# Kernel tuning notes

Measured on AMD Instinct MI355X. Metric: run time of the kernel, lower is better.

## Reference

```python
import jax, jax.numpy as jnp
import numpy as np

NC = 10      # num_classes
HID = 64     # hidden_layer_dim
CIN = 512    # input_channels
THRESH = 100 # _LABEL2MASK_THRESHOL


def setup_inputs() -> dict:
    key = jax.random.key(0)
    k = jax.random.split(key, 5)
    B, h, w = 4, 60, 80
    feature1 = jax.random.normal(k[0], (B, CIN, h, w), jnp.float32)
    feature2 = jax.random.normal(k[1], (B, CIN, h // 2, w // 2), jnp.float32)
    s_in = (2.0 / CIN) ** 0.5   # kaiming_normal_ fan_in for 1x1 conv
    s_h = (2.0 / HID) ** 0.5
    w1 = jax.random.normal(k[2], (HID, CIN), jnp.float32) * s_in
    b1 = jnp.zeros((HID,), jnp.float32)
    w2 = jax.random.normal(k[3], (HID, CIN), jnp.float32) * s_in
    b2 = jnp.zeros((HID,), jnp.float32)
    w3 = jax.random.normal(k[4], (NC + 1, HID), jnp.float32) * s_h
    b3 = jnp.zeros((NC + 1,), jnp.float32)
    return {"feature1": feature1, "feature2": feature2,
            "w1": w1, "b1": b1, "w2": w2, "b2": b2, "w3": w3, "b3": b3}


def _resize_bilinear(x, H, W):
    # torch nn.Upsample(mode='bilinear', align_corners=False) ~ jax.image.resize bilinear
    B, C = x.shape[0], x.shape[1]
    return jax.image.resize(x, (B, C, H, W), method="bilinear")


def _label2bbx(seg):
    # Vectorized replacement of the batch x class Python loop: fused masked
    # min/max reductions per (batch, class). Classes 1..NC-1, class 0 skipped,
    # exactly as in the original. Fixed output shape (B*(NC-1), 6); rows with
    # pixel count < THRESH are filled with -1 (jit-compatible padding).
    B, H, W = seg.shape
    cls = jnp.arange(1, NC)                                   # (NC-1,)
    mask = seg[:, None, :, :] == cls[None, :, None, None]     # (B, NC-1, H, W)
    xs = jnp.arange(W)
    ys = jnp.arange(H)
    count = mask.sum(axis=(-2, -1))                           # (B, NC-1)
    xmin = jnp.min(jnp.where(mask, xs[None, None, None, :], W), axis=(-2, -1))
    xmax = jnp.max(jnp.where(mask, xs[None, None, None, :], -1), axis=(-2, -1))
    ymin = jnp.min(jnp.where(mask, ys[None, None, :, None], H), axis=(-2, -1))
    ymax = jnp.max(jnp.where(mask, ys[None, None, :, None], -1), axis=(-2, -1))
    bids = jnp.broadcast_to(jnp.arange(B)[:, None], (B, NC - 1))
    clsb = jnp.broadcast_to(cls[None, :], (B, NC - 1))
    bbx = jnp.stack([bids, xmin, ymin, xmax, ymax, clsb], axis=-1)  # (B, NC-1, 6)
    valid = (count >= THRESH)[..., None]
    return jnp.where(valid, bbx, -1).reshape(B * (NC - 1), 6)


def reference(feature1, feature2, w1, b1, w2, b2, w3, b3):
    # 1x1 convs expressed as channel GEMMs
    f1 = jax.nn.relu(jnp.einsum('bchw,oc->bohw', feature1, w1) + b1[None, :, None, None])
    f2 = jax.nn.relu(jnp.einsum('bchw,oc->bohw', feature2, w2) + b2[None, :, None, None])
    h, w = feature1.shape[2], feature1.shape[3]
    f2 = _resize_bilinear(f2, h, w)           # Upsample x2
    inter = f1 + f2
    up = _resize_bilinear(inter, 8 * h, 8 * w)  # Upsample x8
    logits = jax.nn.relu(jnp.einsum('bchw,oc->bohw', up, w3) + b3[None, :, None, None])
    probability = jax.nn.softmax(logits, axis=1)   # Softmax2d = softmax over C
    segmentation = jnp.argmax(probability, axis=1)  # (B, H, W)
    bbx = _label2bbx(segmentation)
    return probability, segmentation, bbx
```

## Files before the change

kernel.cpp:

```cpp
#include <hip/hip_runtime.h>

#define DEVINL __device__ __forceinline__

namespace {

constexpr int NB   = 4;
constexpr int CINv = 512;
constexpr int HIDv = 64;
constexpr int NCl  = 11;
constexpr int h1v = 60, w1v = 80;
constexpr int h2v = 30, w2v = 40;
constexpr int Hf = 480, Wf = 640;
constexpr int PPB1 = h1v * w1v;
constexpr int PPB2 = h2v * w2v;
constexpr int NP1 = NB * PPB1;
constexpr int NP2 = NB * PPB2;
constexpr int PPBF = Hf * Wf;
constexpr int NPF = NB * PPBF;

constexpr size_t WS_P1  = 0;
constexpr size_t WS_P2  = WS_P1 + 2ull * HIDv * NP1;
constexpr size_t WS_Z   = WS_P2 + 2ull * HIDv * NP2;
constexpr size_t WS_BBX = WS_Z + (size_t)NB * NCl * PPB1;

constexpr size_t OUT_SEG = (size_t)NB * NCl * PPBF;
constexpr size_t OUT_BBX = OUT_SEG + (size_t)NPF;

DEVINL int iclamp(int v, int lo, int hi) { return v < lo ? lo : (v > hi ? hi : v); }

template <int PPB>
DEVINL void gemm_tile(const float* __restrict__ F, const float* __restrict__ Wt,
                      float* __restrict__ P, int npix, int tile, int khalf,
                      float* A_lds , float* W_lds ) {
  const int t = threadIdx.x;
  const int pg = t & 15;
  const int og = t >> 4;
  const int gp0 = tile * 64;
  const int c0 = khalf * 256;

  float acc[4][4];
#pragma unroll
  for (int i = 0; i < 4; ++i)
#pragma unroll
    for (int j = 0; j < 4; ++j) acc[i][j] = 0.f;

  for (int kb = 0; kb < 8; ++kb) {
    const int cb = c0 + kb * 32;
    __syncthreads();
#pragma unroll
    for (int e = 0; e < 8; ++e) {
      int idx = e * 256 + t;
      int cc = idx >> 6, px = idx & 63;
      int gp = gp0 + px;
      int b = gp / PPB, pb = gp % PPB;
      A_lds[idx] = F[((size_t)b * CINv + (cb + cc)) * PPB + pb];
    }
#pragma unroll
    for (int e = 0; e < 8; ++e) {
      int idx = e * 256 + t;
      int o = idx >> 5, cc = idx & 31;
      W_lds[cc * 68 + o] = Wt[o * CINv + cb + cc];
    }
    __syncthreads();
#pragma unroll
    for (int cc = 0; cc < 32; ++cc) {
      float4 a = *reinterpret_cast<const float4*>(&A_lds[cc * 64 + pg * 4]);
      float4 w = *reinterpret_cast<const float4*>(&W_lds[cc * 68 + og * 4]);
      float av[4] = {a.x, a.y, a.z, a.w};
      float wv[4] = {w.x, w.y, w.z, w.w};
#pragma unroll
      for (int i = 0; i < 4; ++i)
#pragma unroll
        for (int j = 0; j < 4; ++j)
          acc[i][j] = fmaf(av[i], wv[j], acc[i][j]);
    }
  }
#pragma unroll
  for (int j = 0; j < 4; ++j) {
    int o = og * 4 + j;
    float4 v;
    v.x = acc[0][j]; v.y = acc[1][j]; v.z = acc[2][j]; v.w = acc[3][j];
    *reinterpret_cast<float4*>(&P[((size_t)khalf * HIDv + o) * npix + gp0 + pg * 4]) = v;
  }
}

__global__ __launch_bounds__(256) void k_gemm(const float* __restrict__ f1,
                                              const float* __restrict__ f2,
                                              const float* __restrict__ w1,
                                              const float* __restrict__ w2,
                                              float* __restrict__ ws) {
  __shared__ float A_lds[32 * 64];
  __shared__ float W_lds[32 * 68];
  const int bid = blockIdx.x;

  if (bid == 0 && threadIdx.x < 180) {
    int f = threadIdx.x % 5;
    int v = (f == 0) ? 0 : ((f == 1 || f == 3) ? 0x7fffffff : (int)0x80000000);
    reinterpret_cast<int*>(ws + WS_BBX)[threadIdx.x] = v;
  }

  if (bid < 600) {
    gemm_tile<PPB1>(f1, w1, ws + WS_P1, NP1, bid >> 1, bid & 1, A_lds, W_lds);
  } else {
    int tt = bid - 600;
    gemm_tile<PPB2>(f2, w2, ws + WS_P2, NP2, tt >> 1, tt & 1, A_lds, W_lds);
  }
}

__global__ __launch_bounds__(256) void k_combine_z(const float* __restrict__ ws_ro,
                                                   float* __restrict__ ws,
                                                   const float* __restrict__ b1,
                                                   const float* __restrict__ b2,
                                                   const float* __restrict__ w3,
                                                   const float* __restrict__ b3) {
  __shared__ float inter[64 * 64];
  const int t = threadIdx.x;
  const int pxl = t & 63;
  const int qi = t >> 6;
  const int gp = blockIdx.x * 64 + pxl;
  const int b = gp / PPB1, pb = gp % PPB1;
  const int y = pb / w1v, x = pb % w1v;

  const float sx = x * 0.5f - 0.25f;
  const float x0f = floorf(sx);
  const float fx = sx - x0f;
  const int ix0 = iclamp((int)x0f, 0, w2v - 1);
  const int ix1 = iclamp((int)x0f + 1, 0, w2v - 1);
  const float sy = y * 0.5f - 0.25f;
  const float y0f = floorf(sy);
  const float fy = sy - y0f;
  const int iy0 = iclamp((int)y0f, 0, h2v - 1);
  const int iy1 = iclamp((int)y0f + 1, 0, h2v - 1);

  const float* p1 = ws_ro + WS_P1;
  const float* p2 = ws_ro + WS_P2;
  const int base2 = b * PPB2;
  const int i00 = base2 + iy0 * w2v + ix0;
  const int i01 = base2 + iy0 * w2v + ix1;
  const int i10 = base2 + iy1 * w2v + ix0;
  const int i11 = base2 + iy1 * w2v + ix1;

#pragma unroll
  for (int cc = 0; cc < 16; ++cc) {
    const int ch = qi * 16 + cc;
    float v = p1[(size_t)ch * NP1 + gp] + p1[(size_t)(HIDv + ch) * NP1 + gp] + b1[ch];
    v = fmaxf(v, 0.f);
    const float* pa = p2 + (size_t)ch * NP2;
    const float* pbp = p2 + (size_t)(HIDv + ch) * NP2;
    const float bb = b2[ch];
    float v00 = fmaxf(pa[i00] + pbp[i00] + bb, 0.f);
    float v01 = fmaxf(pa[i01] + pbp[i01] + bb, 0.f);
    float v10 = fmaxf(pa[i10] + pbp[i10] + bb, 0.f);
    float v11 = fmaxf(pa[i11] + pbp[i11] + bb, 0.f);
    float top = v00 + fx * (v01 - v00);
    float bot = v10 + fx * (v11 - v10);
    v += top + fy * (bot - top);
    inter[ch * 64 + pxl] = v;
  }
  __syncthreads();

  const int o0 = qi * 3;
  const int ocnt = (qi == 3) ? 2 : 3;
  float* z = ws + WS_Z;
  for (int oo = 0; oo < ocnt; ++oo) {
    const int o = o0 + oo;
    float acc = b3[o];
#pragma unroll
    for (int ch = 0; ch < 64; ++ch)
      acc = fmaf(inter[ch * 64 + pxl], w3[o * HIDv + ch], acc);
    z[((size_t)b * NCl + o) * PPB1 + pb] = acc;
  }
}

__global__ __launch_bounds__(256) void k_up_softmax(const float* __restrict__ ws,
                                                    float* __restrict__ out,
                                                    int* __restrict__ bbxAcc) {
  __shared__ int sCnt[10], sXmin[10], sXmax[10], sYmin[10], sYmax[10];
  const int t = threadIdx.x;
  if (t < 10) {
    sCnt[t] = 0;
    sXmin[t] = 0x7fffffff; sXmax[t] = (int)0x80000000;
    sYmin[t] = 0x7fffffff; sYmax[t] = (int)0x80000000;
  }
  __syncthreads();

  const unsigned fp = ((unsigned)blockIdx.x * 256u + (unsigned)t) * 4u;
  const int b = fp / PPBF;
  const int r = fp % PPBF;
  const int Y = r / Wf, X = r % Wf;

  const float sy = (Y + 0.5f) * 0.125f - 0.5f;
  const float y0f = floorf(sy);
  const float fy = sy - y0f;
  const int iy0 = iclamp((int)y0f, 0, h1v - 1);
  const int iy1 = iclamp((int)y0f + 1, 0, h1v - 1);

  const float sx0 = (X + 0.5f) * 0.125f - 0.5f;
  const float x0f = floorf(sx0);
  const int ix0 = iclamp((int)x0f, 0, w1v - 1);
  const int ix1 = iclamp((int)x0f + 1, 0, w1v - 1);
  float fxk[4];
#pragma unroll
  for (int k = 0; k < 4; ++k) fxk[k] = (X + k + 0.5f) * 0.125f - 0.5f - x0f;

  const float* zb = ws + WS_Z + (size_t)b * NCl * PPB1;
  float lg[NCl][4];
#pragma unroll
  for (int c = 0; c < NCl; ++c) {
    const float* zc = zb + (size_t)c * PPB1;
    float v00 = zc[iy0 * w1v + ix0], v01 = zc[iy0 * w1v + ix1];
    float v10 = zc[iy1 * w1v + ix0], v11 = zc[iy1 * w1v + ix1];
    float l0 = v00 + fy * (v10 - v00);
    float l1 = v01 + fy * (v11 - v01);
#pragma unroll
    for (int k = 0; k < 4; ++k)
      lg[c][k] = fmaxf(l0 + fxk[k] * (l1 - l0), 0.f);
  }

  int bestc[4];
#pragma unroll
  for (int k = 0; k < 4; ++k) {
    float m = lg[0][k];
#pragma unroll
    for (int c = 1; c < NCl; ++c) m = fmaxf(m, lg[c][k]);
    float s = 0.f;
#pragma unroll
    for (int c = 0; c < NCl; ++c) {
      float e = __expf(lg[c][k] - m);
      lg[c][k] = e;
      s += e;
    }
    const float inv = 1.0f / s;
    float bp = -1.f;
    int bi = 0;
#pragma unroll
    for (int c = 0; c < NCl; ++c) {
      float p = lg[c][k] * inv;
      lg[c][k] = p;
      if (p > bp) { bp = p; bi = c; }
    }
    bestc[k] = bi;
  }

  float* prob = out + (size_t)b * NCl * PPBF;
#pragma unroll
  for (int c = 0; c < NCl; ++c) {
    float4 v;
    v.x = lg[c][0]; v.y = lg[c][1]; v.z = lg[c][2]; v.w = lg[c][3];
    *reinterpret_cast<float4*>(&prob[(size_t)c * PPBF + r]) = v;
  }
  {
    float4 v;
    v.x = (float)bestc[0]; v.y = (float)bestc[1];
    v.z = (float)bestc[2]; v.w = (float)bestc[3];
    *reinterpret_cast<float4*>(&out[OUT_SEG + fp]) = v;
  }

  for (int c = 1; c <= 9; ++c) {
    int cnt = 0, mnx = 0x7fffffff, mxx = (int)0x80000000;
#pragma unroll
    for (int k = 0; k < 4; ++k)
      if (bestc[k] == c) { ++cnt; mnx = min(mnx, X + k); mxx = max(mxx, X + k); }
    if (cnt) {
      atomicAdd(&sCnt[c], cnt);
      atomicMin(&sXmin[c], mnx);
      atomicMax(&sXmax[c], mxx);
      atomicMin(&sYmin[c], Y);
      atomicMax(&sYmax[c], Y);
    }
  }
  __syncthreads();
  if (t >= 1 && t <= 9 && sCnt[t] > 0) {
    int* e = bbxAcc + (b * 9 + (t - 1)) * 5;
    atomicAdd(e + 0, sCnt[t]);
    atomicMin(e + 1, sXmin[t]);
    atomicMax(e + 2, sXmax[t]);
    atomicMin(e + 3, sYmin[t]);
    atomicMax(e + 4, sYmax[t]);
  }
}

__global__ void k_bbx_final(const int* __restrict__ acc, float* __restrict__ out) {
  const int t = threadIdx.x;
  if (t >= 36) return;
  const int* e = acc + t * 5;
  float* o = out + OUT_BBX + t * 6;
  if (e[0] >= 100) {
    o[0] = (float)(t / 9);
    o[1] = (float)e[1];
    o[2] = (float)e[3];
    o[3] = (float)e[2];
    o[4] = (float)e[4];
    o[5] = (float)(t % 9 + 1);
  } else {
    for (int i = 0; i < 6; ++i) o[i] = -1.f;
  }
}

}

extern "C" void kernel_launch(void* const* d_in, const int* in_sizes, int n_in,
                              void* d_out, int out_size, void* d_ws, size_t ws_size,
                              hipStream_t stream) {
  const float* f1 = (const float*)d_in[0];
  const float* f2 = (const float*)d_in[1];
  const float* w1 = (const float*)d_in[2];
  const float* b1 = (const float*)d_in[3];
  const float* w2 = (const float*)d_in[4];
  const float* b2 = (const float*)d_in[5];
  const float* w3 = (const float*)d_in[6];
  const float* b3 = (const float*)d_in[7];
  float* out = (float*)d_out;
  float* ws = (float*)d_ws;

  hipLaunchKernelGGL(k_gemm, dim3(750), dim3(256), 0, stream, f1, f2, w1, w2, ws);
  hipLaunchKernelGGL(k_combine_z, dim3(300), dim3(256), 0, stream, ws, ws, b1, b2, w3, b3);
  hipLaunchKernelGGL(k_up_softmax, dim3(1200), dim3(256), 0, stream, ws, out,
                     (int*)(ws + WS_BBX));
  hipLaunchKernelGGL(k_bbx_final, dim3(1), dim3(64), 0, stream,
                     (const int*)(ws + WS_BBX), out);
}
```

Baseline: 85.72 us.

## Tile upsample-softmax blocks in 2D and stage low-res logits in LDS

Each block of the final upsample+softmax kernel now covers a 128x8 pixel tile. The block first loads the 11-channel 3x18 low-resolution logit neighbourhood into shared memory, and bilinear taps then read from LDS instead of scattered global loads. The argmax is taken on the pre-softmax logits rather than on the normalised probabilities, and the reciprocal uses the hardware rcp builtin. The cost is an extra LDS fill and barrier per block, plus slightly different rounding and tie behaviour.

```diff
diff --git a/kernel.cpp b/kernel.cpp
--- a/kernel.cpp
+++ b/kernel.cpp
@@ -175,41 +175,55 @@
 __global__ __launch_bounds__(256) void k_up_softmax(const float* __restrict__ ws,
                                                     float* __restrict__ out,
                                                     int* __restrict__ bbxAcc) {
+  constexpr int ZR = 3, ZC = 18, ZN = NCl * ZR * ZC;
+  __shared__ float zt[ZN];
   __shared__ int sCnt[10], sXmin[10], sXmax[10], sYmin[10], sYmax[10];
+
   const int t = threadIdx.x;
+  const int tile = blockIdx.x;
+  const int tx = tile % 5;
+  const int ty = (tile / 5) % 60;
+  const int b  = tile / 300;
+
+  const int base_x = tx * 16 - 1;
+  const int base_y = ty - 1;
+
   if (t < 10) {
     sCnt[t] = 0;
     sXmin[t] = 0x7fffffff; sXmax[t] = (int)0x80000000;
     sYmin[t] = 0x7fffffff; sYmax[t] = (int)0x80000000;
   }
+  const float* zb = ws + WS_Z + (size_t)b * NCl * PPB1;
+  for (int e = t; e < ZN; e += 256) {
+    int ch = e / (ZR * ZC);
+    int rc = e % (ZR * ZC);
+    int row = rc / ZC, col = rc % ZC;
+    int gr = iclamp(base_y + row, 0, h1v - 1);
+    int gc = iclamp(base_x + col, 0, w1v - 1);
+    zt[e] = zb[(size_t)ch * PPB1 + gr * w1v + gc];
+  }
   __syncthreads();
 
-  const unsigned fp = ((unsigned)blockIdx.x * 256u + (unsigned)t) * 4u;
-  const int b = fp / PPBF;
-  const int r = fp % PPBF;
-  const int Y = r / Wf, X = r % Wf;
-
-  const float sy = (Y + 0.5f) * 0.125f - 0.5f;
-  const float y0f = floorf(sy);
-  const float fy = sy - y0f;
-  const int iy0 = iclamp((int)y0f, 0, h1v - 1);
-  const int iy1 = iclamp((int)y0f + 1, 0, h1v - 1);
-
-  const float sx0 = (X + 0.5f) * 0.125f - 0.5f;
-  const float x0f = floorf(sx0);
-  const int ix0 = iclamp((int)x0f, 0, w1v - 1);
-  const int ix1 = iclamp((int)x0f + 1, 0, w1v - 1);
+  const int xg = t & 31;
+  const int yr = t >> 5;
+  const int X = tx * 128 + xg * 4;
+  const int Y = ty * 8 + yr;
+  const int r = Y * Wf + X;
+
+  const int lcx0 = (xg + 1) >> 1;
+  const int lry0 = (yr >= 4) ? 1 : 0;
+  const float fy = (Y + 0.5f) * 0.125f - 0.5f - (float)(base_y + lry0);
   float fxk[4];
 #pragma unroll
-  for (int k = 0; k < 4; ++k) fxk[k] = (X + k + 0.5f) * 0.125f - 0.5f - x0f;
-
-  const float* zb = ws + WS_Z + (size_t)b * NCl * PPB1;
+  for (int k = 0; k < 4; ++k)
+    fxk[k] = (X + k + 0.5f) * 0.125f - 0.5f - (float)(base_x + lcx0);
+
   float lg[NCl][4];
 #pragma unroll
   for (int c = 0; c < NCl; ++c) {
-    const float* zc = zb + (size_t)c * PPB1;
-    float v00 = zc[iy0 * w1v + ix0], v01 = zc[iy0 * w1v + ix1];
-    float v10 = zc[iy1 * w1v + ix0], v11 = zc[iy1 * w1v + ix1];
+    const int base = c * (ZR * ZC) + lry0 * ZC + lcx0;
+    float v00 = zt[base],       v01 = zt[base + 1];
+    float v10 = zt[base + ZC],  v11 = zt[base + ZC + 1];
     float l0 = v00 + fy * (v10 - v00);
     float l1 = v01 + fy * (v11 - v01);
 #pragma unroll
@@ -221,8 +235,12 @@
 #pragma unroll
   for (int k = 0; k < 4; ++k) {
     float m = lg[0][k];
-#pragma unroll
-    for (int c = 1; c < NCl; ++c) m = fmaxf(m, lg[c][k]);
+    int bi = 0;
+#pragma unroll
+    for (int c = 1; c < NCl; ++c) {
+      if (lg[c][k] > m) { m = lg[c][k]; bi = c; }
+    }
+    bestc[k] = bi;
     float s = 0.f;
 #pragma unroll
     for (int c = 0; c < NCl; ++c) {
@@ -230,16 +248,9 @@
       lg[c][k] = e;
       s += e;
     }
-    const float inv = 1.0f / s;
-    float bp = -1.f;
-    int bi = 0;
-#pragma unroll
-    for (int c = 0; c < NCl; ++c) {
-      float p = lg[c][k] * inv;
-      lg[c][k] = p;
-      if (p > bp) { bp = p; bi = c; }
-    }
-    bestc[k] = bi;
+    const float inv = __builtin_amdgcn_rcpf(s);
+#pragma unroll
+    for (int c = 0; c < NCl; ++c) lg[c][k] *= inv;
   }
 
   float* prob = out + (size_t)b * NCl * PPBF;
@@ -253,7 +264,7 @@
     float4 v;
     v.x = (float)bestc[0]; v.y = (float)bestc[1];
     v.z = (float)bestc[2]; v.w = (float)bestc[3];
-    *reinterpret_cast<float4*>(&out[OUT_SEG + fp]) = v;
+    *reinterpret_cast<float4*>(&out[OUT_SEG + (size_t)b * PPBF + r]) = v;
   }
 
   for (int c = 1; c <= 9; ++c) {
```

Result: no change. 86.09 us (+0.4%).
